# Optimization experiments

Measured on AMD Instinct MI355X. Metric: run time of the kernel, lower is better.

The kernel has to match this reference:

```python
import jax, jax.numpy as jnp
import numpy as np

D_MODEL = 512
N_HEADS = 8
D_K = D_MODEL // N_HEADS
MAX_LEN = 512  # max_seq_len; rel table has 2*MAX_LEN-1 rows


def setup_inputs() -> dict:
    key = jax.random.key(0)
    ks = jax.random.split(key, 7)
    B, S = 8, 512
    s = 1.0 / np.sqrt(D_MODEL)
    return {
        "x": jax.random.normal(ks[0], (B, S, D_MODEL), jnp.float32),
        "Wq": jax.random.normal(ks[1], (D_MODEL, D_MODEL), jnp.float32) * s,
        "bq": jnp.zeros((D_MODEL,), jnp.float32),
        "Wk": jax.random.normal(ks[2], (D_MODEL, D_MODEL), jnp.float32) * s,
        "bk": jnp.zeros((D_MODEL,), jnp.float32),
        "Wv": jax.random.normal(ks[3], (D_MODEL, D_MODEL), jnp.float32) * s,
        "bv": jnp.zeros((D_MODEL,), jnp.float32),
        "Wo": jax.random.normal(ks[4], (D_MODEL, D_MODEL), jnp.float32) * s,
        "bo": jnp.zeros((D_MODEL,), jnp.float32),
        "rel_embed": jax.random.normal(ks[5], (2 * MAX_LEN - 1, D_MODEL), jnp.float32) * 0.02,
    }


def reference(x, Wq, bq, Wk, bk, Wv, bv, Wo, bo, rel_embed):
    B, S, _ = x.shape
    scale = np.sqrt(D_K).astype(np.float32)

    def split_heads(t):  # (B,S,D) -> (B,H,S,dk)
        return t.reshape(B, S, N_HEADS, D_K).transpose(0, 2, 1, 3)

    q = split_heads(x @ Wq.T + bq)
    k = split_heads(x @ Wk.T + bk)
    v = split_heads(x @ Wv.T + bv)

    scores = jnp.einsum('bhqd,bhkd->bhqk', q, k) / scale

    # relative position bias: idx[q_pos, k_pos] = k_pos - q_pos + MAX_LEN - 1
    pos = jnp.arange(S)
    rel_idx = pos[None, :] - pos[:, None] + (MAX_LEN - 1)  # (S,S)
    rel_bias = rel_embed[rel_idx].reshape(S, S, N_HEADS, D_K)  # (S,S,H,dk)
    scores = scores + jnp.einsum('bhqd,qkhd->bhqk', q, rel_bias)

    attn = jax.nn.softmax(scores, axis=-1)
    out = jnp.einsum('bhqk,bhkd->bhqd', attn, v)  # (B,H,S,dk)
    out = out.transpose(0, 2, 1, 3).reshape(B, S, D_MODEL)
    return out @ Wo.T + bo
```

## Files before the change

### kernel.cpp

```cpp
#include <hip/hip_runtime.h>
#include <math.h>

#define B_  8
#define S_  512
#define D_  512
#define H_  8
#define DK_ 64

typedef __attribute__((ext_vector_type(8))) short short8;
typedef __attribute__((ext_vector_type(4))) float f32x4;

#define MFMA_BF16(a, b, c) __builtin_amdgcn_mfma_f32_16x16x32_bf16(a, b, c, 0, 0, 0)

__device__ __forceinline__ unsigned bf16_rne(float x) {
    unsigned u = __float_as_uint(x);
    return (u + 0x7FFFu + ((u >> 16) & 1u)) >> 16;
}
__device__ __forceinline__ float bf16f(unsigned h) { return __uint_as_float(h << 16); }

__device__ __forceinline__ void glds16(const ushort* g, ushort* l) {
    __builtin_amdgcn_global_load_lds(
        (const __attribute__((address_space(1))) unsigned int*)g,
        (__attribute__((address_space(3))) unsigned int*)l,
        16, 0, 0);
}

__global__ __launch_bounds__(256)
void conv_pl(const float* __restrict__ x,
             const float* __restrict__ wq, const float* __restrict__ wk,
             const float* __restrict__ wv, const float* __restrict__ wo,
             ushort* __restrict__ Xh, ushort* __restrict__ Xl,
             ushort* __restrict__ Wqh, ushort* __restrict__ Wql,
             ushort* __restrict__ Wkh, ushort* __restrict__ Wkl,
             ushort* __restrict__ Wvh, ushort* __restrict__ Wvl,
             ushort* __restrict__ Woh, ushort* __restrict__ Wol) {
    const int bid = blockIdx.x;
    const float* src; ushort* dh; ushort* dl; int i4;
    if (bid < 2048) {
        src = x; dh = Xh; dl = Xl; i4 = bid * 256 + threadIdx.x;
    } else {
        const int r = bid - 2048;
        const int wsel = r >> 8;
        src = (wsel == 0) ? wq : (wsel == 1) ? wk : (wsel == 2) ? wv : wo;
        dh  = (wsel == 0) ? Wqh : (wsel == 1) ? Wkh : (wsel == 2) ? Wvh : Woh;
        dl  = (wsel == 0) ? Wql : (wsel == 1) ? Wkl : (wsel == 2) ? Wvl : Wol;
        i4 = (r & 255) * 256 + threadIdx.x;
    }
    const float4 v = ((const float4*)src)[i4];
    unsigned h[4], l[4];
    const float* vp = &v.x;
    #pragma unroll
    for (int j = 0; j < 4; ++j) { h[j] = bf16_rne(vp[j]); l[j] = bf16_rne(vp[j] - bf16f(h[j])); }
    ((uint2*)dh)[i4] = make_uint2(h[0] | (h[1] << 16), h[2] | (h[3] << 16));
    ((uint2*)dl)[i4] = make_uint2(l[0] | (l[1] << 16), l[2] | (l[3] << 16));
}

__global__ __launch_bounds__(256)
void conv_rel(const float* __restrict__ rel, ushort* __restrict__ Rg) {
    const int idx = blockIdx.x * 256 + threadIdx.x;
    const int d2 = idx & 31;
    const int rr = (idx >> 5) % 1152;
    const int h  = idx / (1152 * 32);
    unsigned v0 = 0, v1 = 0;
    if (rr >= 64 && rr < 64 + 1023) {
        const float* s = &rel[(size_t)(rr - 64) * 512 + h * 64 + d2 * 2];
        v0 = bf16_rne(s[0]); v1 = bf16_rne(s[1]);
    }
    *(uint*)&Rg[((size_t)h * 1152 + rr) * 64 + d2 * 2] = v0 | (v1 << 16);
}

template<int XB, int OM>
__global__ __launch_bounds__(256, 2)
void gemm_mfma(const ushort* __restrict__ Xhp, const ushort* __restrict__ Xlp,
               const ushort* __restrict__ Yh0, const ushort* __restrict__ Yl0,
               const ushort* __restrict__ Yh1, const ushort* __restrict__ Yl1,
               const float* __restrict__ bias0, const float* __restrict__ bias1,
               float* __restrict__ outF,
               ushort* __restrict__ oh0, ushort* __restrict__ ol0,
               ushort* __restrict__ oh1, ushort* __restrict__ ol1) {
    __shared__ ushort Xs[2][2][64 * 64];
    __shared__ ushort Ys[2][2][64 * 64];

    const int z = blockIdx.z;
    const ushort* Yhp = z ? Yh1 : Yh0;
    const ushort* Ylp = z ? Yl1 : Yl0;
    const float*  bias = z ? bias1 : bias0;
    ushort* ohp = z ? oh1 : oh0;
    ushort* olp = z ? ol1 : ol0;

    const int tid = threadIdx.x;
    const int w = tid >> 6, lane = tid & 63;
    const int g = lane >> 4, c = lane & 15;
    const int rloc = lane >> 3, cc8 = lane & 7;
    const int cp = cc8 ^ rloc;
    const int r0 = blockIdx.y * 64;
    const int c0 = blockIdx.x * 64;

    const f32x4 fz = {0.f, 0.f, 0.f, 0.f};
    f32x4 acc[2][2] = {{fz, fz}, {fz, fz}};

    auto stage = [&](int kt, int buf) {
        const int k0 = kt * 64;
        const ushort* gb; ushort* lb; size_t rstr;
        if (w < 2) {
            const ushort* Xp = (w == 1) ? Xlp : Xhp;
            if (XB == 0) { gb = Xp + (size_t)r0 * 512 + k0; rstr = 512; }
            else {
                const int b = r0 >> 9, s0 = r0 & 511, h = k0 >> 6;
                gb = Xp + (((size_t)(b * 8 + h)) * 512 + s0) * 64; rstr = 64;
            }
            lb = &Xs[buf][w][0];
        } else {
            gb = ((w == 2) ? Yhp : Ylp) + (size_t)c0 * 512 + k0; rstr = 512;
            lb = &Ys[buf][w - 2][0];
        }
        #pragma unroll
        for (int j = 0; j < 8; ++j)
            glds16(gb + (size_t)(j * 8 + rloc) * rstr + cp * 8, lb + j * 512);
    };

    auto compute = [&](int buf) {
        #pragma unroll
        for (int ks = 0; ks < 2; ++ks) {
            short8 axh[2], axl[2], byh[2], byl[2];
            const int wm = (w >> 1) * 32, wn = (w & 1) * 32;
            #pragma unroll
            for (int t = 0; t < 2; ++t) {
                int row = wm + t * 16 + c;
                int off = row * 64 + (((ks * 4 + g) ^ (row & 7)) * 8);
                axh[t] = *(const short8*)&Xs[buf][0][off];
                axl[t] = *(const short8*)&Xs[buf][1][off];
                row = wn + t * 16 + c;
                off = row * 64 + (((ks * 4 + g) ^ (row & 7)) * 8);
                byh[t] = *(const short8*)&Ys[buf][0][off];
                byl[t] = *(const short8*)&Ys[buf][1][off];
            }
            #pragma unroll
            for (int tm = 0; tm < 2; ++tm)
                #pragma unroll
                for (int tn = 0; tn < 2; ++tn) {
                    acc[tm][tn] = MFMA_BF16(axh[tm], byh[tn], acc[tm][tn]);
                    acc[tm][tn] = MFMA_BF16(axl[tm], byh[tn], acc[tm][tn]);
                    acc[tm][tn] = MFMA_BF16(axh[tm], byl[tn], acc[tm][tn]);
                }
        }
    };

    stage(0, 0);
    __syncthreads();
    for (int kt = 0; kt < 8; ++kt) {
        if (kt < 7) stage(kt + 1, (kt + 1) & 1);
        compute(kt & 1);
        __syncthreads();
    }

    const int wm = (w >> 1) * 32, wn = (w & 1) * 32;
    if (OM == 0) {
        #pragma unroll
        for (int tn = 0; tn < 2; ++tn) {
            const int gc = c0 + wn + tn * 16 + c;
            const float bv = bias[gc];
            #pragma unroll
            for (int tm = 0; tm < 2; ++tm)
                #pragma unroll
                for (int i = 0; i < 4; ++i) {
                    const int gr = r0 + wm + tm * 16 + g * 4 + i;
                    outF[(size_t)gr * 512 + gc] = acc[tm][tn][i] + bv;
                }
        }
    } else if (OM == 2) {
        #pragma unroll
        for (int tn = 0; tn < 2; ++tn) {
            const int gc = c0 + wn + tn * 16 + c;
            const int h = gc >> 6, dk = gc & 63;
            const float bv = bias[gc];
            #pragma unroll
            for (int tm = 0; tm < 2; ++tm)
                #pragma unroll
                for (int i = 0; i < 4; ++i) {
                    const int gr = r0 + wm + tm * 16 + g * 4 + i;
                    const int b = gr >> 9, s = gr & 511;
                    const float v = acc[tm][tn][i] + bv;
                    const unsigned hb = bf16_rne(v);
                    const size_t a = (((size_t)(b * 8 + h)) * 512 + s) * 64 + dk;
                    ohp[a] = (ushort)hb;
                    olp[a] = (ushort)bf16_rne(v - bf16f(hb));
                }
        }
    } else {
        #pragma unroll
        for (int tm = 0; tm < 2; ++tm)
            #pragma unroll
            for (int i = 0; i < 4; ++i) {
                const int gr = r0 + wm + tm * 16 + g * 4 + i;
                const int h = gr >> 6, dk = gr & 63;
                const float bv = bias[gr];
                #pragma unroll
                for (int tn = 0; tn < 2; ++tn) {
                    const int gc = c0 + wn + tn * 16 + c;
                    const int b = gc >> 9, s = gc & 511;
                    const float v = acc[tm][tn][i] + bv;
                    const unsigned hb = bf16_rne(v);
                    const size_t a = (((size_t)(b * 8 + h)) * 64 + dk) * 512 + s;
                    ohp[a] = (ushort)hb;
                    olp[a] = (ushort)bf16_rne(v - bf16f(hb));
                }
            }
    }
}

__global__ __launch_bounds__(256, 2)
void attn_mfma(const ushort* __restrict__ Qhp, const ushort* __restrict__ Qlp,
               const ushort* __restrict__ Khp, const ushort* __restrict__ Klp,
               const ushort* __restrict__ Vhp, const ushort* __restrict__ Vlp,
               const ushort* __restrict__ Rg,
               ushort* __restrict__ Oh, ushort* __restrict__ Ol) {
    __shared__ ushort Ksm[2][64 * 64];
    __shared__ ushort Vsm[2][64 * 64];
    __shared__ float  Psm[4][16 * 64];

    const int tid  = threadIdx.x;
    const int w    = tid >> 6;
    const int lane = tid & 63;
    const int g    = lane >> 4;
    const int c    = lane & 15;
    const int rloc = lane >> 3, cc8 = lane & 7;
    const int cp   = cc8 ^ rloc;
    const int bh   = blockIdx.y;
    const int h    = bh & 7;
    const int qw   = blockIdx.x * 64 + w * 16;

    short8 qfh[2], qfl[2];
    #pragma unroll
    for (int ks = 0; ks < 2; ++ks) {
        const size_t qi = ((size_t)bh * 512 + qw + c) * 64 + ks * 32 + g * 8;
        qfh[ks] = *(const short8*)&Qhp[qi];
        qfl[ks] = *(const short8*)&Qlp[qi];
    }

    const f32x4 fz = {0.f, 0.f, 0.f, 0.f};
    f32x4 o[4] = {fz, fz, fz, fz};
    float mreg[4], lreg[4];
    #pragma unroll
    for (int i = 0; i < 4; ++i) { mreg[i] = -INFINITY; lreg[i] = 0.f; }

    const ushort* KhB = Khp + (size_t)bh * 512 * 64;
    const ushort* KlB = Klp + (size_t)bh * 512 * 64;
    const ushort* VhB = Vhp + (size_t)bh * 64 * 512;
    const ushort* VlB = Vlp + (size_t)bh * 64 * 512;

    for (int kt = 0; kt < 8; ++kt) {
        const int k0 = kt * 64;
        __syncthreads();
        {
            const ushort* gb; ushort* lb; size_t rstr;
            if (w == 0)      { gb = KhB + (size_t)k0 * 64; lb = &Ksm[0][0]; rstr = 64; }
            else if (w == 1) { gb = KlB + (size_t)k0 * 64; lb = &Ksm[1][0]; rstr = 64; }
            else if (w == 2) { gb = VhB + k0;              lb = &Vsm[0][0]; rstr = 512; }
            else             { gb = VlB + k0;              lb = &Vsm[1][0]; rstr = 512; }
            #pragma unroll
            for (int j = 0; j < 8; ++j)
                glds16(gb + (size_t)(j * 8 + rloc) * rstr + cp * 8, lb + j * 512);
        }
        __syncthreads();

        f32x4 u[5];
        #pragma unroll
        for (int ut = 0; ut < 5; ++ut) u[ut] = fz;
        const int rrow0 = k0 - qw + 559 + c;
        #pragma unroll
        for (int ks = 0; ks < 2; ++ks)
            #pragma unroll
            for (int ut = 0; ut < 5; ++ut) {
                const short8 rf = *(const short8*)
                    &Rg[((size_t)h * 1152 + rrow0 + ut * 16) * 64 + ks * 32 + g * 8];
                u[ut] = MFMA_BF16(qfh[ks], rf, u[ut]);
            }

        f32x4 s[4];
        #pragma unroll
        for (int tc = 0; tc < 4; ++tc) s[tc] = fz;
        #pragma unroll
        for (int ks = 0; ks < 2; ++ks)
            #pragma unroll
            for (int tc = 0; tc < 4; ++tc) {
                const int row = tc * 16 + c;
                const int chv = ((ks * 4 + g) ^ (row & 7)) * 8;
                const short8 kh8 = *(const short8*)&Ksm[0][row * 64 + chv];
                const short8 kl8 = *(const short8*)&Ksm[1][row * 64 + chv];
                s[tc] = MFMA_BF16(qfh[ks], kh8, s[tc]);
                s[tc] = MFMA_BF16(qfl[ks], kh8, s[tc]);
                s[tc] = MFMA_BF16(qfh[ks], kl8, s[tc]);
            }

        #pragma unroll
        for (int i = 0; i < 4; ++i) {
            const int r = g * 4 + i;
            const int srcl = (g << 4) | ((c - r) & 15);
            float sv[4];
            #pragma unroll
            for (int tc = 0; tc < 4; ++tc) {
                const float va = __shfl(u[tc + 1][i], srcl);
                const float vb = __shfl(u[tc][i], srcl);
                sv[tc] = s[tc][i] * 0.125f + ((c >= r) ? va : vb);
            }
            float tm = fmaxf(fmaxf(sv[0], sv[1]), fmaxf(sv[2], sv[3]));
            tm = fmaxf(tm, __shfl_xor(tm, 1));
            tm = fmaxf(tm, __shfl_xor(tm, 2));
            tm = fmaxf(tm, __shfl_xor(tm, 4));
            tm = fmaxf(tm, __shfl_xor(tm, 8));
            const float mold = mreg[i];
            const float mn = fmaxf(mold, tm);
            const float corr = __expf(mold - mn);
            mreg[i] = mn;
            float lacc = lreg[i] * corr;
            #pragma unroll
            for (int dt = 0; dt < 4; ++dt) o[dt][i] *= corr;
            #pragma unroll
            for (int tc = 0; tc < 4; ++tc) {
                const float p = __expf(sv[tc] - mn);
                lacc += p;
                const int col = tc * 16 + c;
                Psm[w][r * 64 + (((col >> 2) ^ r) << 2) + (col & 3)] = p;
            }
            lreg[i] = lacc;
        }
        asm volatile("s_waitcnt lgkmcnt(0)" ::: "memory");

        #pragma unroll
        for (int ks = 0; ks < 2; ++ks) {
            const int pc0 = ks * 8 + g * 2;
            const f32x4 pa = *(const f32x4*)&Psm[w][c * 64 + ((pc0 ^ c) << 2)];
            const f32x4 pb = *(const f32x4*)&Psm[w][c * 64 + (((pc0 + 1) ^ c) << 2)];
            short8 aph, apl;
            #pragma unroll
            for (int j = 0; j < 8; ++j) {
                const float pj = (j < 4) ? pa[j] : pb[j - 4];
                const unsigned hbits = bf16_rne(pj);
                aph[j] = (short)hbits;
                apl[j] = (short)bf16_rne(pj - bf16f(hbits));
            }
            #pragma unroll
            for (int dt = 0; dt < 4; ++dt) {
                const int row = dt * 16 + c;
                const int chv = ((ks * 4 + g) ^ (row & 7)) * 8;
                const short8 vh8 = *(const short8*)&Vsm[0][row * 64 + chv];
                const short8 vl8 = *(const short8*)&Vsm[1][row * 64 + chv];
                o[dt] = MFMA_BF16(aph, vh8, o[dt]);
                o[dt] = MFMA_BF16(aph, vl8, o[dt]);
                o[dt] = MFMA_BF16(apl, vh8, o[dt]);
            }
        }
    }

    #pragma unroll
    for (int i = 0; i < 4; ++i) {
        float ls = lreg[i];
        ls += __shfl_xor(ls, 1);
        ls += __shfl_xor(ls, 2);
        ls += __shfl_xor(ls, 4);
        ls += __shfl_xor(ls, 8);
        const float inv = 1.0f / ls;
        const int r = g * 4 + i;
        #pragma unroll
        for (int dt = 0; dt < 4; ++dt) {
            const float val = o[dt][i] * inv;
            const unsigned hb = bf16_rne(val);
            const size_t a = ((size_t)bh * 512 + qw + r) * 64 + dt * 16 + c;
            Oh[a] = (ushort)hb;
            Ol[a] = (ushort)bf16_rne(val - bf16f(hb));
        }
    }
}

extern "C" void kernel_launch(void* const* d_in, const int* in_sizes, int n_in,
                              void* d_out, int out_size, void* d_ws, size_t ws_size,
                              hipStream_t stream) {
    const float* x   = (const float*)d_in[0];
    const float* Wq  = (const float*)d_in[1];
    const float* bq  = (const float*)d_in[2];
    const float* Wk  = (const float*)d_in[3];
    const float* bk  = (const float*)d_in[4];
    const float* Wv  = (const float*)d_in[5];
    const float* bv  = (const float*)d_in[6];
    const float* Wo  = (const float*)d_in[7];
    const float* bo  = (const float*)d_in[8];
    const float* rel = (const float*)d_in[9];
    float* out = (float*)d_out;

    const size_t NP = (size_t)B_ * H_ * S_ * DK_;
    const size_t WP = (size_t)D_ * D_;
    ushort* Xh  = (ushort*)d_ws;
    ushort* Xl  = Xh + NP;
    ushort* Wqh = Xl + NP;
    ushort* Wql = Wqh + WP;
    ushort* Wkh = Wql + WP;
    ushort* Wkl = Wkh + WP;
    ushort* Wvh = Wkl + WP;
    ushort* Wvl = Wvh + WP;
    ushort* Woh = Wvl + WP;
    ushort* Wol = Woh + WP;
    ushort* Qh  = Wol + WP;
    ushort* Ql  = Qh + NP;
    ushort* Kh  = Ql + NP;
    ushort* Kl  = Kh + NP;
    ushort* Vh  = Kl + NP;
    ushort* Vl  = Vh + NP;
    ushort* Rg  = Vl + NP;

    conv_pl<<<3072, 256, 0, stream>>>(x, Wq, Wk, Wv, Wo,
                                      Xh, Xl, Wqh, Wql, Wkh, Wkl, Wvh, Wvl, Woh, Wol);
    conv_rel<<<1152, 256, 0, stream>>>(rel, Rg);

    gemm_mfma<0, 2><<<dim3(8, 64, 2), 256, 0, stream>>>(
        Xh, Xl, Wqh, Wql, Wkh, Wkl, bq, bk, nullptr, Qh, Ql, Kh, Kl);
    gemm_mfma<0, 3><<<dim3(64, 8, 1), 256, 0, stream>>>(
        Wvh, Wvl, Xh, Xl, nullptr, nullptr, bv, nullptr, nullptr, Vh, Vl, nullptr, nullptr);

    attn_mfma<<<dim3(8, 64), 256, 0, stream>>>(Qh, Ql, Kh, Kl, Vh, Vl, Rg, Xh, Xl);

    gemm_mfma<1, 0><<<dim3(8, 64, 1), 256, 0, stream>>>(
        Xh, Xl, Woh, Wol, nullptr, nullptr, bo, nullptr, out, nullptr, nullptr, nullptr, nullptr);
}
```

Baseline: 101.8 us.

## Split attention over key halves with combine kernel and drop V low-part

```diff
diff --git a/kernel.cpp b/kernel.cpp
--- a/kernel.cpp
+++ b/kernel.cpp
@@ -200,23 +200,21 @@
                     const int gc = c0 + wn + tn * 16 + c;
                     const int b = gc >> 9, s = gc & 511;
                     const float v = acc[tm][tn][i] + bv;
-                    const unsigned hb = bf16_rne(v);
                     const size_t a = (((size_t)(b * 8 + h)) * 64 + dk) * 512 + s;
-                    ohp[a] = (ushort)hb;
-                    olp[a] = (ushort)bf16_rne(v - bf16f(hb));
+                    ohp[a] = (ushort)bf16_rne(v);
                 }
             }
     }
 }
 
-__global__ __launch_bounds__(256, 2)
+__global__ __launch_bounds__(256, 4)
 void attn_mfma(const ushort* __restrict__ Qhp, const ushort* __restrict__ Qlp,
                const ushort* __restrict__ Khp, const ushort* __restrict__ Klp,
-               const ushort* __restrict__ Vhp, const ushort* __restrict__ Vlp,
-               const ushort* __restrict__ Rg,
-               ushort* __restrict__ Oh, ushort* __restrict__ Ol) {
+               const ushort* __restrict__ Vhp, const ushort* __restrict__ Rg,
+               float* __restrict__ Op0, float* __restrict__ Op1,
+               float2* __restrict__ Ml0, float2* __restrict__ Ml1) {
     __shared__ ushort Ksm[2][64 * 64];
-    __shared__ ushort Vsm[2][64 * 64];
+    __shared__ ushort Vsm[64 * 64];
     __shared__ float  Psm[4][16 * 64];
 
     const int tid  = threadIdx.x;
@@ -228,7 +226,11 @@
     const int cp   = cc8 ^ rloc;
     const int bh   = blockIdx.y;
     const int h    = bh & 7;
+    const int z    = blockIdx.z;
     const int qw   = blockIdx.x * 64 + w * 16;
+
+    float* __restrict__ Op = z ? Op1 : Op0;
+    float2* __restrict__ Ml = z ? Ml1 : Ml0;
 
     short8 qfh[2], qfl[2];
     #pragma unroll
@@ -247,20 +249,22 @@
     const ushort* KhB = Khp + (size_t)bh * 512 * 64;
     const ushort* KlB = Klp + (size_t)bh * 512 * 64;
     const ushort* VhB = Vhp + (size_t)bh * 64 * 512;
-    const ushort* VlB = Vlp + (size_t)bh * 64 * 512;
-
-    for (int kt = 0; kt < 8; ++kt) {
+
+    for (int kt = z * 4; kt < z * 4 + 4; ++kt) {
         const int k0 = kt * 64;
         __syncthreads();
-        {
-            const ushort* gb; ushort* lb; size_t rstr;
-            if (w == 0)      { gb = KhB + (size_t)k0 * 64; lb = &Ksm[0][0]; rstr = 64; }
-            else if (w == 1) { gb = KlB + (size_t)k0 * 64; lb = &Ksm[1][0]; rstr = 64; }
-            else if (w == 2) { gb = VhB + k0;              lb = &Vsm[0][0]; rstr = 512; }
-            else             { gb = VlB + k0;              lb = &Vsm[1][0]; rstr = 512; }
+        if (w < 2) {
+            const ushort* gb = (w == 0 ? KhB : KlB) + (size_t)k0 * 64;
+            ushort* lb = &Ksm[w][0];
             #pragma unroll
             for (int j = 0; j < 8; ++j)
-                glds16(gb + (size_t)(j * 8 + rloc) * rstr + cp * 8, lb + j * 512);
+                glds16(gb + (size_t)(j * 8 + rloc) * 64 + cp * 8, lb + j * 512);
+        } else {
+            const ushort* gb = VhB + k0 + (size_t)(w - 2) * 32 * 512;
+            ushort* lb = &Vsm[(w - 2) * 32 * 64];
+            #pragma unroll
+            for (int j = 0; j < 4; ++j)
+                glds16(gb + (size_t)(j * 8 + rloc) * 512 + cp * 8, lb + j * 512);
         }
         __syncthreads();
 
@@ -344,10 +348,8 @@
             for (int dt = 0; dt < 4; ++dt) {
                 const int row = dt * 16 + c;
                 const int chv = ((ks * 4 + g) ^ (row & 7)) * 8;
-                const short8 vh8 = *(const short8*)&Vsm[0][row * 64 + chv];
-                const short8 vl8 = *(const short8*)&Vsm[1][row * 64 + chv];
+                const short8 vh8 = *(const short8*)&Vsm[row * 64 + chv];
                 o[dt] = MFMA_BF16(aph, vh8, o[dt]);
-                o[dt] = MFMA_BF16(aph, vl8, o[dt]);
                 o[dt] = MFMA_BF16(apl, vh8, o[dt]);
             }
         }
@@ -360,16 +362,42 @@
         ls += __shfl_xor(ls, 2);
         ls += __shfl_xor(ls, 4);
         ls += __shfl_xor(ls, 8);
-        const float inv = 1.0f / ls;
         const int r = g * 4 + i;
-        #pragma unroll
-        for (int dt = 0; dt < 4; ++dt) {
-            const float val = o[dt][i] * inv;
-            const unsigned hb = bf16_rne(val);
-            const size_t a = ((size_t)bh * 512 + qw + r) * 64 + dt * 16 + c;
-            Oh[a] = (ushort)hb;
-            Ol[a] = (ushort)bf16_rne(val - bf16f(hb));
-        }
+        const size_t rowi = (size_t)bh * 512 + qw + r;
+        if (c == 0) Ml[rowi] = make_float2(mreg[i], ls);
+        #pragma unroll
+        for (int dt = 0; dt < 4; ++dt)
+            Op[rowi * 64 + dt * 16 + c] = o[dt][i];
+    }
+}
+
+__global__ __launch_bounds__(256)
+void attn_combine(const float* __restrict__ Op0, const float* __restrict__ Op1,
+                  const float2* __restrict__ Ml0, const float2* __restrict__ Ml1,
+                  ushort* __restrict__ Oh, ushort* __restrict__ Ol) {
+    const int tid = threadIdx.x;
+    const int row = blockIdx.x * 64 + (tid >> 2);
+    const int d0 = (tid & 3) * 16;
+    const float2 a = Ml0[row], b = Ml1[row];
+    const float m = fmaxf(a.x, b.x);
+    float w0 = __expf(a.x - m), w1 = __expf(b.x - m);
+    const float inv = 1.0f / (a.y * w0 + b.y * w1);
+    w0 *= inv; w1 *= inv;
+    const size_t base = (size_t)row * 64 + d0;
+    #pragma unroll
+    for (int j = 0; j < 4; ++j) {
+        const float4 v0 = *(const float4*)&Op0[base + j * 4];
+        const float4 v1 = *(const float4*)&Op1[base + j * 4];
+        float vv[4] = {v0.x * w0 + v1.x * w1, v0.y * w0 + v1.y * w1,
+                       v0.z * w0 + v1.z * w1, v0.w * w0 + v1.w * w1};
+        unsigned hb[4], lb4[4];
+        #pragma unroll
+        for (int q = 0; q < 4; ++q) {
+            hb[q] = bf16_rne(vv[q]);
+            lb4[q] = bf16_rne(vv[q] - bf16f(hb[q]));
+        }
+        *(uint2*)&Oh[base + j * 4] = make_uint2(hb[0] | (hb[1] << 16), hb[2] | (hb[3] << 16));
+        *(uint2*)&Ol[base + j * 4] = make_uint2(lb4[0] | (lb4[1] << 16), lb4[2] | (lb4[3] << 16));
     }
 }
 
@@ -405,8 +433,11 @@
     ushort* Kh  = Ql + NP;
     ushort* Kl  = Kh + NP;
     ushort* Vh  = Kl + NP;
-    ushort* Vl  = Vh + NP;
-    ushort* Rg  = Vl + NP;
+    ushort* Rg  = Vh + NP;
+    float*  Op1 = (float*)(Rg + 589824);
+    float2* Ml0 = (float2*)(Op1 + NP);
+    float2* Ml1 = Ml0 + 32768;
+    float*  Op0 = (float*)d_ws;
 
     conv_pl<<<3072, 256, 0, stream>>>(x, Wq, Wk, Wv, Wo,
                                       Xh, Xl, Wqh, Wql, Wkh, Wkl, Wvh, Wvl, Woh, Wol);
@@ -415,10 +446,13 @@
     gemm_mfma<0, 2><<<dim3(8, 64, 2), 256, 0, stream>>>(
         Xh, Xl, Wqh, Wql, Wkh, Wkl, bq, bk, nullptr, Qh, Ql, Kh, Kl);
     gemm_mfma<0, 3><<<dim3(64, 8, 1), 256, 0, stream>>>(
-        Wvh, Wvl, Xh, Xl, nullptr, nullptr, bv, nullptr, nullptr, Vh, Vl, nullptr, nullptr);
-
-    attn_mfma<<<dim3(8, 64), 256, 0, stream>>>(Qh, Ql, Kh, Kl, Vh, Vl, Rg, Xh, Xl);
+        Wvh, Wvl, Xh, Xl, nullptr, nullptr, bv, nullptr, nullptr, Vh, nullptr, nullptr, nullptr);
+
+    attn_mfma<<<dim3(8, 64, 2), 256, 0, stream>>>(
+        Qh, Ql, Kh, Kl, Vh, Rg, Op0, Op1, Ml0, Ml1);
+
+    attn_combine<<<512, 256, 0, stream>>>(Op0, Op1, Ml0, Ml1, Kh, Kl);
 
     gemm_mfma<1, 0><<<dim3(8, 64, 1), 256, 0, stream>>>(
-        Xh, Xl, Woh, Wol, nullptr, nullptr, bo, nullptr, out, nullptr, nullptr, nullptr, nullptr);
-}
+        Kh, Kl, Woh, Wol, nullptr, nullptr, bo, nullptr, out, nullptr, nullptr, nullptr, nullptr);
+}
```

Result: slower. 107.9 us (+6.0%).
